# Performance work log

Measured on AMD Instinct MI355X. Metric: run time of the kernel, lower is better.

## Reference

```python
import jax, jax.numpy as jnp
import numpy as np

N, E, HN, K = 4096, 8192, 1024, 8
NF, EF = 128, 64
NH = [256, 256]
EH = [64, 64]
EMB = NH[-1] + len(EH)  # 258
BN_EPS = 1e-5


def setup_inputs() -> dict:
    key = jax.random.key(0)
    ks = jax.random.split(key, 16)

    def nrm(k, shape, fan):
        return jax.random.normal(k, shape, jnp.float32) / np.float32(np.sqrt(fan))

    return {
        "X_n": jax.random.normal(ks[0], (N, NF), jnp.float32),
        "X_e": jax.random.normal(ks[1], (E, EF), jnp.float32),
        # row-normalized-ish adjacency and scaled Laplacian to keep activations bounded
        "A_tilde": jax.random.uniform(ks[2], (N, N), jnp.float32) / np.float32(N),
        "L1_tilde": jax.random.normal(ks[3], (E, E), jnp.float32) / np.float32(np.sqrt(E)),
        "B1": jax.random.normal(ks[4], (N, E), jnp.float32) / np.float32(np.sqrt(E)),
        # GNN params (Linear stores weight as [out, in])
        "gnn_W1": nrm(ks[5], (NH[0], NF), NF), "gnn_b1": jnp.zeros((NH[0],), jnp.float32),
        "gnn_W2": nrm(ks[6], (NH[1], NH[0]), NH[0]), "gnn_b2": jnp.zeros((NH[1],), jnp.float32),
        # HoSC layer 1: in=EF, out=EH[0]
        "hosc_W1": nrm(ks[7], (EH[0], EF), EF), "hosc_b1": jnp.zeros((EH[0],), jnp.float32),
        "bn1_g": jnp.ones((EH[0],), jnp.float32), "bn1_b": jnp.zeros((EH[0],), jnp.float32),
        # HoSC layer 2: in=1 (after channel-max), out=EH[1]
        "hosc_W2": nrm(ks[8], (EH[1], 1), 1), "hosc_b2": jnp.zeros((EH[1],), jnp.float32),
        "bn2_g": jnp.ones((EH[1],), jnp.float32), "bn2_b": jnp.zeros((EH[1],), jnp.float32),
        # heads
        "node_W": nrm(ks[9], (1, EMB), EMB), "node_b": jnp.zeros((1,), jnp.float32),
        "edge_W": nrm(ks[10], (1, len(EH)), len(EH)), "edge_b": jnp.zeros((1,), jnp.float32),
        "hyper_W": nrm(ks[11], (1, EMB), EMB), "hyper_b": jnp.zeros((1,), jnp.float32),
        "hyperedges": jax.random.randint(ks[12], (HN, K), 0, N, jnp.int64),
    }


def _bn(x, g, b):
    # training-mode BatchNorm1d: biased batch statistics over rows
    m = jnp.mean(x, axis=0)
    v = jnp.var(x, axis=0)
    return g * (x - m) / jnp.sqrt(v + BN_EPS) + b


def _hosc_layer(Z, L1, W, bias, g, b):
    Zt = Z @ W.T + bias            # [E, out]
    Zc = L1 @ Zt                   # [E, out]
    Zp = jax.nn.relu(_bn(Zc, g, b))
    return jnp.max(Zp, axis=1, keepdims=True)  # [E, 1]


def reference(X_n, X_e, A_tilde, L1_tilde, B1,
              gnn_W1, gnn_b1, gnn_W2, gnn_b2,
              hosc_W1, hosc_b1, bn1_g, bn1_b,
              hosc_W2, hosc_b2, bn2_g, bn2_b,
              node_W, node_b, edge_W, edge_b, hyper_W, hyper_b,
              hyperedges):
    # --- GNN over nodes ---
    H = jax.nn.relu((A_tilde @ X_n) @ gnn_W1.T + gnn_b1)   # [N, 256]
    H_n = jax.nn.relu((A_tilde @ H) @ gnn_W2.T + gnn_b2)   # [N, 256]

    # --- HoSC over edges ---
    Z1 = _hosc_layer(X_e, L1_tilde, hosc_W1, hosc_b1, bn1_g, bn1_b)  # [E, 1]
    Z2 = _hosc_layer(Z1, L1_tilde, hosc_W2, hosc_b2, bn2_g, bn2_b)   # [E, 1]
    Z_H = jnp.concatenate([Z1, Z2], axis=1)                 # [E, 2]

    # --- fuse edge info into nodes ---
    H_e = B1 @ Z_H                                          # [N, 2]
    Hcat = jnp.concatenate([H_n, H_e], axis=1)              # [N, 258]

    node_prob = jax.nn.sigmoid(Hcat @ node_W.T + node_b).squeeze(-1)  # [N]
    edge_prob = jax.nn.sigmoid(Z_H @ edge_W.T + edge_b).squeeze(-1)   # [E]

    # vectorized hyperedge gather-mean-linear-sigmoid (fixed-size hyperedges)
    hfeat = Hcat[hyperedges].mean(axis=1)                   # [HN, 258]
    hyperedge_prob = jax.nn.sigmoid(hfeat @ hyper_W.T + hyper_b)  # [HN, 1]

    return node_prob, edge_prob, hyperedge_prob, Hcat
```

## Files before the change

kernel.cpp:

```cpp
#include <hip/hip_runtime.h>
#include <hip/hip_bf16.h>

using f32x4  = __attribute__((ext_vector_type(4))) float;
using u32x4  = __attribute__((ext_vector_type(4))) unsigned int;
using bf16x8 = __attribute__((ext_vector_type(8))) short;

__device__ __forceinline__ ushort f2bf(float x) {
    union { __hip_bfloat16 h; ushort u; } cv;
    cv.h = __float2bfloat16(x);
    return cv.u;
}
__device__ __forceinline__ unsigned pk2(float lo, float hi) {
    return (unsigned)f2bf(lo) | ((unsigned)f2bf(hi) << 16);
}
__device__ __forceinline__ float sigmoidf_(float x) { return 1.f / (1.f + expf(-x)); }

template<int NSUM, bool A_BF16, bool ABR, bool SPLIT, bool RELU, bool BF16_OUT, bool HAS_BIAS>
__device__ __forceinline__ void gemm_body(
    ushort* As, ushort* Bs,
    const void* __restrict__ Avoid, const ushort* __restrict__ B,
    const float* __restrict__ abias, const float* __restrict__ bias,
    float* __restrict__ Cf, ushort* __restrict__ Cb,
    int M, int N, int K, int ldc, int kPerChunk, long pStride,
    int bx, int by, int bz)
{
    const int tid  = threadIdx.x;
    const int lane = tid & 63;
    const int wid  = tid >> 6;
    const int wr   = wid >> 1, wc = wid & 1;
    const int g    = lane >> 4, lr = lane & 15;
    const long m0  = (long)bx * 128;
    const int  n0  = by * 64;

    int kbeg = 0, kend = K;
    if (SPLIT) { kbeg = bz * kPerChunk; kend = kbeg + kPerChunk; if (kend > K) kend = K; }

    const int bkr = tid & 31;
    const int bcb = tid >> 5;

    const float*  Af = (const float*)Avoid;
    const ushort* Ab = (const ushort*)Avoid;

    f32x4 pa[4];
    u32x4 pab[2];
    u32x4 pb;

    auto loadT = [&](int k0) {
        if (A_BF16) {
#pragma unroll
            for (int i = 0; i < 2; i++) {
                int s = tid + 256 * i; int row = s >> 2, c8 = s & 3;
                pab[i] = *(const u32x4*)(Ab + (m0 + row) * (long)K + k0 + c8 * 8);
            }
        } else {
#pragma unroll
            for (int i = 0; i < 4; i++) {
                int s = tid + 256 * i; int row = s >> 3, c4 = s & 7;
                const float* base = Af + (m0 + row) * (long)K + k0 + c4 * 4;
                f32x4 v = *(const f32x4*)base;
                if (NSUM > 0) {
#pragma unroll
                    for (int z = 1; z < NSUM; z++) v += *(const f32x4*)(base + z * pStride);
                }
                if (ABR) {
                    f32x4 bq = *(const f32x4*)(abias + k0 + c4 * 4);
                    v.x = fmaxf(v.x + bq.x, 0.f);
                    v.y = fmaxf(v.y + bq.y, 0.f);
                    v.z = fmaxf(v.z + bq.z, 0.f);
                    v.w = fmaxf(v.w + bq.w, 0.f);
                }
                pa[i] = v;
            }
        }
        pb = *(const u32x4*)(B + (long)(k0 + bkr) * N + n0 + bcb * 8);
    };
    auto storeT = [&]() {
        if (A_BF16) {
#pragma unroll
            for (int i = 0; i < 2; i++) {
                int s = tid + 256 * i; int row = s >> 2, c8 = s & 3;
                *(u32x4*)(&As[row * 40 + c8 * 8]) = pab[i];
            }
        } else {
#pragma unroll
            for (int i = 0; i < 4; i++) {
                int s = tid + 256 * i; int row = s >> 3, c4 = s & 7;
                ushort4 w;
                w.x = f2bf(pa[i].x); w.y = f2bf(pa[i].y);
                w.z = f2bf(pa[i].z); w.w = f2bf(pa[i].w);
                *(ushort4*)(&As[row * 40 + c4 * 4]) = w;
            }
        }
        const ushort* p8 = (const ushort*)&pb;
#pragma unroll
        for (int j = 0; j < 8; j++) Bs[(bcb * 8 + j) * 40 + bkr] = p8[j];
    };

    f32x4 acc[4][2] = {};

    const int nk = (kend - kbeg) >> 5;
    loadT(kbeg);
    for (int t = 0; t < nk; ++t) {
        storeT();
        __syncthreads();
        if (t + 1 < nk) loadT(kbeg + ((t + 1) << 5));
        bf16x8 af[4], bfr[2];
#pragma unroll
        for (int fm = 0; fm < 4; fm++)
            af[fm] = *(const bf16x8*)(&As[(wr * 64 + fm * 16 + lr) * 40 + g * 8]);
#pragma unroll
        for (int fn = 0; fn < 2; fn++)
            bfr[fn] = *(const bf16x8*)(&Bs[(wc * 32 + fn * 16 + lr) * 40 + g * 8]);
#pragma unroll
        for (int fm = 0; fm < 4; fm++)
#pragma unroll
            for (int fn = 0; fn < 2; fn++)
                acc[fm][fn] = __builtin_amdgcn_mfma_f32_16x16x32_bf16(af[fm], bfr[fn], acc[fm][fn], 0, 0, 0);
        __syncthreads();
    }

    if (SPLIT) {
        float* P = Cf + (long)bz * M * N;
#pragma unroll
        for (int fm = 0; fm < 4; fm++)
#pragma unroll
            for (int fn = 0; fn < 2; fn++)
#pragma unroll
                for (int rr = 0; rr < 4; rr++) {
                    long row = m0 + wr * 64 + fm * 16 + g * 4 + rr;
                    int  col = n0 + wc * 32 + fn * 16 + lr;
                    P[row * N + col] = acc[fm][fn][rr];
                }
    } else {
#pragma unroll
        for (int fm = 0; fm < 4; fm++)
#pragma unroll
            for (int fn = 0; fn < 2; fn++)
#pragma unroll
                for (int rr = 0; rr < 4; rr++) {
                    long row = m0 + wr * 64 + fm * 16 + g * 4 + rr;
                    int  col = n0 + wc * 32 + fn * 16 + lr;
                    float v = acc[fm][fn][rr];
                    if (HAS_BIAS) v += bias[col];
                    if (RELU) v = fmaxf(v, 0.f);
                    if (BF16_OUT) Cb[row * ldc + col] = f2bf(v);
                    else          Cf[row * ldc + col] = v;
                }
    }
}

__global__ __launch_bounds__(256)
void prep_k(const float* __restrict__ A, ushort* __restrict__ Abf,
            const float* __restrict__ Xn, const float* __restrict__ W1, ushort* __restrict__ T1,
            const float* __restrict__ Xe, const float* __restrict__ Wh,
            const float* __restrict__ hb, ushort* __restrict__ Zt1,
            const float* __restrict__ W2, ushort* __restrict__ W2t,
            float* __restrict__ stats)
{
    __shared__ float xs[1024];
    int b = blockIdx.x, t = threadIdx.x;
    if (b < 8192) {
        long j = (long)b * 256 + t;
        f32x4 v0 = ((const f32x4*)A)[2 * j];
        f32x4 v1 = ((const f32x4*)A)[2 * j + 1];
        u32x4 w;
        w.x = pk2(v0.x, v0.y); w.y = pk2(v0.z, v0.w);
        w.z = pk2(v1.x, v1.y); w.w = pk2(v1.z, v1.w);
        ((u32x4*)Abf)[j] = w;
    } else if (b < 8704) {
        int r0 = (b - 8192) * 8;
        for (int idx = t; idx < 1024; idx += 256) xs[idx] = Xn[(long)r0 * 128 + idx];
        __syncthreads();
        float acc[8] = {};
        const float* wrow = W1 + (long)t * 128;
        for (int i = 0; i < 128; i++) {
            float w = wrow[i];
#pragma unroll
            for (int r = 0; r < 8; r++) acc[r] += xs[r * 128 + i] * w;
        }
#pragma unroll
        for (int r = 0; r < 8; r++) T1[(long)(r0 + r) * 256 + t] = f2bf(acc[r]);
    } else if (b < 10752) {
        int row = (b - 8704) * 4 + (t >> 6);
        int o   = t & 63;
        const float* xr = Xe + (long)row * 64;
        const float* wr = Wh + (long)o * 64;
        float acc = hb[o];
#pragma unroll 8
        for (int i = 0; i < 64; i++) acc += xr[i] * wr[i];
        Zt1[(long)row * 64 + o] = f2bf(acc);
    } else if (b < 11008) {
        int j = (b - 10752) * 256 + t;
        int i = j >> 8, o = j & 255;
        W2t[j] = f2bf(W2[o * 256 + i]);
    } else {
        if (t < 256) stats[t] = 0.f;
    }
}

__device__ __forceinline__ void bnred_body(int b, const float* __restrict__ P,
                                           float* __restrict__ Zc,
                                           float* __restrict__ pstats,
                                           float* __restrict__ gsum, float* __restrict__ gsq,
                                           unsigned* __restrict__ ctr)
{
    const long MN = 8192 * 64;
    int t = threadIdx.x;
    int c = t & 63, rg = t >> 6;
    float sx = 0.f, sq = 0.f;
    int base = b * 32 + rg;
#pragma unroll 4
    for (int i = 0; i < 8; i++) {
        long idx = (long)(base + 4 * i) * 64 + c;
        float x = 0.f;
#pragma unroll
        for (int z = 0; z < 8; z++) x += P[idx + z * MN];
        Zc[idx] = x;
        sx += x; sq += x * x;
    }
    __shared__ float ls[256], lq[256];
    ls[t] = sx; lq[t] = sq;
    __syncthreads();
    if (t < 64) {
        float a = ls[t] + ls[t + 64] + ls[t + 128] + ls[t + 192];
        float q = lq[t] + lq[t + 64] + lq[t + 128] + lq[t + 192];
        pstats[b * 128 + t]      = a;
        pstats[b * 128 + 64 + t] = q;
    }
    __threadfence();
    __syncthreads();
    __shared__ unsigned lastflag;
    if (t == 0) {
        unsigned old = atomicAdd(ctr, 1u);
        lastflag = (old == 255u);
    }
    __syncthreads();
    if (lastflag) {
        __threadfence();
        if (t < 128) {
            float a = 0.f;
            for (int bb = 0; bb < 256; bb++) a += pstats[bb * 128 + t];
            if (t < 64) gsum[t] = a;
            else        gsq[t - 64] = a;
        }
    }
}

__device__ __forceinline__ void z1_body(int b, const float* __restrict__ Zc,
                                        const float* __restrict__ gsum, const float* __restrict__ gsq,
                                        const float* __restrict__ g, const float* __restrict__ bb,
                                        float* __restrict__ Z1)
{
    int w = threadIdx.x >> 6, lane = threadIdx.x & 63;
    int row = b * 4 + w;
    const float inv = 1.f / 8192.f;
    float m = gsum[lane] * inv;
    float v = gsq[lane] * inv - m * m;
    float x = Zc[row * 64 + lane];
    float y = fmaxf(g[lane] * (x - m) * rsqrtf(v + 1e-5f) + bb[lane], 0.f);
#pragma unroll
    for (int o = 32; o > 0; o >>= 1) y = fmaxf(y, __shfl_xor(y, o));
    if (lane == 0) Z1[row] = y;
}

__device__ __forceinline__ void pass2_body(int row, const float* __restrict__ L1,
                                           const float* __restrict__ Z1,
                                           float* __restrict__ s, float* __restrict__ r)
{
    int t = threadIdx.x;
    int l = t & 63, w = t >> 6;
    const f32x4* rp = (const f32x4*)(L1 + (long)row * 8192);
    const f32x4* z4 = (const f32x4*)Z1;
    float as = 0.f, ar = 0.f;
#pragma unroll 4
    for (int k = 0; k < 8; k++) {
        f32x4 v = rp[t + 256 * k];
        f32x4 z = z4[t + 256 * k];
        as += v.x * z.x + v.y * z.y + v.z * z.z + v.w * z.w;
        ar += v.x + v.y + v.z + v.w;
    }
#pragma unroll
    for (int o = 32; o > 0; o >>= 1) { as += __shfl_xor(as, o); ar += __shfl_xor(ar, o); }
    __shared__ float sw[4], rw[4];
    if (l == 0) { sw[w] = as; rw[w] = ar; }
    __syncthreads();
    if (t == 0) {
        s[row] = sw[0] + sw[1] + sw[2] + sw[3];
        r[row] = rw[0] + rw[1] + rw[2] + rw[3];
    }
}

__device__ __forceinline__ void hcatred_body(int b, const float* __restrict__ P,
                                             const float* __restrict__ b2, float* __restrict__ hcat)
{
    const long MNq = (long)4096 * 256 / 4;
    int j = b * 256 + threadIdx.x;
    int row = j >> 6, c4 = (j & 63) * 4;
    const f32x4* Q = (const f32x4*)P;
    f32x4 v = Q[j] + Q[j + MNq] + Q[j + 2 * MNq] + Q[j + 3 * MNq];
    f32x4 bq = *(const f32x4*)(b2 + c4);
    float* dst = hcat + (long)row * 258 + c4;
    float2 lo = { fmaxf(v.x + bq.x, 0.f), fmaxf(v.y + bq.y, 0.f) };
    float2 hi = { fmaxf(v.z + bq.z, 0.f), fmaxf(v.w + bq.w, 0.f) };
    *(float2*)dst = lo;
    *(float2*)(dst + 2) = hi;
}

__global__ __launch_bounds__(256)
void dual_a_k(const float* __restrict__ L1, const ushort* __restrict__ Zt1, float* __restrict__ Pa,
              const ushort* __restrict__ Abf, const ushort* __restrict__ T1, float* __restrict__ Pb)
{
    __shared__ ushort As[128 * 40];
    __shared__ ushort Bs[64 * 40];
    int bid = blockIdx.x;
    if (bid < 512) {
        gemm_body<0, false, false, true, false, false, false>(
            As, Bs, L1, Zt1, nullptr, nullptr, Pa, nullptr,
            8192, 64, 8192, 64, 1024, 0, bid & 63, 0, bid >> 6);
    } else {
        int b = bid - 512;
        gemm_body<0, true, false, true, false, false, false>(
            As, Bs, Abf, T1, nullptr, nullptr, Pb, nullptr,
            4096, 256, 4096, 256, 1024, 0, b & 31, (b >> 5) & 3, b >> 7);
    }
}

__global__ __launch_bounds__(256)
void dual_b_k(const float* __restrict__ Pb, const float* __restrict__ gb1,
              const ushort* __restrict__ W2t, ushort* __restrict__ T2,
              const float* __restrict__ Pa, float* __restrict__ Zc1,
              float* __restrict__ pstats,
              float* __restrict__ gsum, float* __restrict__ gsq, unsigned* __restrict__ ctr)
{
    __shared__ ushort As[128 * 40];
    __shared__ ushort Bs[64 * 40];
    int bid = blockIdx.x;
    if (bid < 128) {
        gemm_body<4, false, true, false, false, true, false>(
            As, Bs, Pb, W2t, gb1, nullptr, nullptr, T2,
            4096, 256, 256, 256, 0, (long)4096 * 256, bid & 31, bid >> 5, 0);
    } else {
        bnred_body(bid - 128, Pa, Zc1, pstats, gsum, gsq, ctr);
    }
}

__global__ __launch_bounds__(256)
void dual_c_k(const ushort* __restrict__ Abf, const ushort* __restrict__ T2, float* __restrict__ Pa,
              const float* __restrict__ Zc1, const float* __restrict__ gsum,
              const float* __restrict__ gsq, const float* __restrict__ bn1g,
              const float* __restrict__ bn1b, float* __restrict__ Z1)
{
    __shared__ ushort As[128 * 40];
    __shared__ ushort Bs[64 * 40];
    int bid = blockIdx.x;
    if (bid < 512) {
        gemm_body<0, true, false, true, false, false, false>(
            As, Bs, Abf, T2, nullptr, nullptr, Pa, nullptr,
            4096, 256, 4096, 256, 1024, 0, bid & 31, (bid >> 5) & 3, bid >> 7);
    } else {
        z1_body(bid - 512, Zc1, gsum, gsq, bn1g, bn1b, Z1);
    }
}

__global__ __launch_bounds__(256)
void dual_d_k(const float* __restrict__ Pa, const float* __restrict__ gb2, float* __restrict__ hcat,
              const float* __restrict__ L1, const float* __restrict__ Z1,
              float* __restrict__ s, float* __restrict__ r)
{
    int bid = blockIdx.x;
    if (bid < 1024) hcatred_body(bid, Pa, gb2, hcat);
    else            pass2_body(bid - 1024, L1, Z1, s, r);
}

__global__ __launch_bounds__(1024) void stats2_k(const float* __restrict__ s, const float* __restrict__ r,
                                                 float* __restrict__ S5)
{
    int t = threadIdx.x, l = t & 63, w = t >> 6;
    float Ss = 0, Sr = 0, Sss = 0, Srr = 0, Ssr = 0;
    for (int i = t; i < 8192; i += 1024) {
        float sv = s[i], rv = r[i];
        Ss += sv; Sr += rv; Sss += sv * sv; Srr += rv * rv; Ssr += sv * rv;
    }
#pragma unroll
    for (int o = 32; o > 0; o >>= 1) {
        Ss += __shfl_xor(Ss, o); Sr += __shfl_xor(Sr, o);
        Sss += __shfl_xor(Sss, o); Srr += __shfl_xor(Srr, o); Ssr += __shfl_xor(Ssr, o);
    }
    __shared__ float buf[16][5];
    if (l == 0) { buf[w][0] = Ss; buf[w][1] = Sr; buf[w][2] = Sss; buf[w][3] = Srr; buf[w][4] = Ssr; }
    __syncthreads();
    if (t < 5) {
        float a = 0.f;
#pragma unroll
        for (int i = 0; i < 16; i++) a += buf[i][t];
        S5[t] = a;
    }
}

__global__ __launch_bounds__(256) void z2_edge_k(const float* __restrict__ s, const float* __restrict__ r,
                                                 const float* __restrict__ S,
                                                 const float* __restrict__ W2, const float* __restrict__ b2,
                                                 const float* __restrict__ g2, const float* __restrict__ bb2,
                                                 const float* __restrict__ eW, const float* __restrict__ eb,
                                                 const float* __restrict__ Z1,
                                                 float* __restrict__ Z2, float* __restrict__ edge_out)
{
    int w = threadIdx.x >> 6, lane = threadIdx.x & 63;
    int row = blockIdx.x * 4 + w;
    const float inv = 1.f / 8192.f;
    float ms = S[0] * inv, mr = S[1] * inv;
    float vs = S[2] * inv - ms * ms;
    float vr = S[3] * inv - mr * mr;
    float cv = S[4] * inv - ms * mr;
    float w2 = W2[lane], bz = b2[lane];
    float mc = w2 * ms + bz * mr;
    float vc = w2 * w2 * vs + 2.f * w2 * bz * cv + bz * bz * vr;
    float x  = w2 * s[row] + bz * r[row];
    float y  = fmaxf(g2[lane] * (x - mc) * rsqrtf(vc + 1e-5f) + bb2[lane], 0.f);
#pragma unroll
    for (int o = 32; o > 0; o >>= 1) y = fmaxf(y, __shfl_xor(y, o));
    if (lane == 0) {
        Z2[row] = y;
        float e = Z1[row] * eW[0] + y * eW[1] + eb[0];
        edge_out[row] = sigmoidf_(e);
    }
}

__global__ __launch_bounds__(256) void he_node_k(const float* __restrict__ B1, const float* __restrict__ Z1,
                                                 const float* __restrict__ Z2, float* __restrict__ hcat,
                                                 const float* __restrict__ nW, const float* __restrict__ nb,
                                                 float* __restrict__ node_out)
{
    int n = blockIdx.x, t = threadIdx.x;
    int l = t & 63, w = t >> 6;
    const f32x4* rp  = (const f32x4*)(B1 + (long)n * 8192);
    const f32x4* z1v = (const f32x4*)Z1;
    const f32x4* z2v = (const f32x4*)Z2;
    float a1 = 0.f, a2 = 0.f;
#pragma unroll 4
    for (int k = 0; k < 8; k++) {
        f32x4 v = rp[t + 256 * k];
        f32x4 p = z1v[t + 256 * k];
        f32x4 q = z2v[t + 256 * k];
        a1 += v.x * p.x + v.y * p.y + v.z * p.z + v.w * p.w;
        a2 += v.x * q.x + v.y * q.y + v.z * q.z + v.w * q.w;
    }
    float d = hcat[(long)n * 258 + t] * nW[t];
#pragma unroll
    for (int o = 32; o > 0; o >>= 1) {
        a1 += __shfl_xor(a1, o); a2 += __shfl_xor(a2, o); d += __shfl_xor(d, o);
    }
    __shared__ float s1[4], s2[4], s3[4];
    if (l == 0) { s1[w] = a1; s2[w] = a2; s3[w] = d; }
    __syncthreads();
    if (t == 0) {
        float A1 = s1[0] + s1[1] + s1[2] + s1[3];
        float A2 = s2[0] + s2[1] + s2[2] + s2[3];
        float D  = s3[0] + s3[1] + s3[2] + s3[3];
        hcat[(long)n * 258 + 256] = A1;
        hcat[(long)n * 258 + 257] = A2;
        node_out[n] = sigmoidf_(D + A1 * nW[256] + A2 * nW[257] + nb[0]);
    }
}

__global__ __launch_bounds__(256) void hyper_k(const void* __restrict__ he_idx,
                                               const float* __restrict__ hcat,
                                               const float* __restrict__ hW, const float* __restrict__ hb,
                                               float* __restrict__ out)
{
    int w = threadIdx.x >> 6, lane = threadIdx.x & 63;
    int h = blockIdx.x * 4 + w;
    const unsigned int* u = (const unsigned int*)he_idx;
    unsigned int odd = u[2 * lane + 1];
    bool is64 = __all(odd == 0u);
    float acc = 0.f;
    for (int k = 0; k < 8; k++) {
        int idx;
        if (is64) idx = (int)((const long long*)he_idx)[h * 8 + k];
        else      idx = ((const int*)he_idx)[h * 8 + k];
        const float* hr = hcat + (long)idx * 258;
        for (int d = lane; d < 258; d += 64) acc += hr[d] * hW[d];
    }
    acc *= 0.125f;
#pragma unroll
    for (int o = 32; o > 0; o >>= 1) acc += __shfl_xor(acc, o);
    if (lane == 0) out[h] = sigmoidf_(acc + hb[0]);
}

extern "C" void kernel_launch(void* const* d_in, const int* in_sizes, int n_in,
                              void* d_out, int out_size, void* d_ws, size_t ws_size,
                              hipStream_t stream)
{
    const float* X_n  = (const float*)d_in[0];
    const float* X_e  = (const float*)d_in[1];
    const float* A_t  = (const float*)d_in[2];
    const float* L1   = (const float*)d_in[3];
    const float* B1   = (const float*)d_in[4];
    const float* gW1  = (const float*)d_in[5];
    const float* gb1  = (const float*)d_in[6];
    const float* gW2  = (const float*)d_in[7];
    const float* gb2  = (const float*)d_in[8];
    const float* hW1  = (const float*)d_in[9];
    const float* hb1  = (const float*)d_in[10];
    const float* bn1g = (const float*)d_in[11];
    const float* bn1b = (const float*)d_in[12];
    const float* hW2  = (const float*)d_in[13];
    const float* hb2  = (const float*)d_in[14];
    const float* bn2g = (const float*)d_in[15];
    const float* bn2b = (const float*)d_in[16];
    const float* nW   = (const float*)d_in[17];
    const float* nb   = (const float*)d_in[18];
    const float* eW   = (const float*)d_in[19];
    const float* ebb  = (const float*)d_in[20];
    const float* yW   = (const float*)d_in[21];
    const float* yb   = (const float*)d_in[22];
    const void*  he   = d_in[23];

    float* out       = (float*)d_out;
    float* out_node  = out;
    float* out_edge  = out + 4096;
    float* out_hyper = out + 12288;
    float* hcat      = out + 13312;

    size_t off = 0;
    auto alloc = [&](size_t bytes) {
        void* p = (char*)d_ws + off;
        off = (off + bytes + 255) & ~(size_t)255;
        return p;
    };
    ushort* Abf    = (ushort*)alloc((size_t)4096 * 4096 * 2);
    ushort* T1     = (ushort*)alloc(4096 * 256 * 2);
    ushort* T2     = (ushort*)alloc(4096 * 256 * 2);
    ushort* Zt1    = (ushort*)alloc(8192 * 64 * 2);
    ushort* W2t    = (ushort*)alloc(256 * 256 * 2);
    float*  Zc1    = (float*)alloc(8192 * 64 * 4);
    float*  stats  = (float*)alloc(256 * 4);
    float*  gsum   = stats;
    float*  gsq    = stats + 64;
    float*  S5     = stats + 128;
    unsigned* ctr  = (unsigned*)(stats + 192);
    float*  pstats = (float*)alloc(256 * 128 * 4);
    float*  Z1     = (float*)alloc(8192 * 4);
    float*  Z2     = (float*)alloc(8192 * 4);
    float*  sbuf   = (float*)alloc(8192 * 4);
    float*  rbuf   = (float*)alloc(8192 * 4);
    float*  Pa     = (float*)alloc((size_t)8192 * 64 * 8 * 4);
    float*  Pb     = (float*)alloc((size_t)4096 * 256 * 4 * 4);

    prep_k<<<11009, 256, 0, stream>>>(A_t, Abf, X_n, gW1, T1, X_e, hW1, hb1, Zt1,
                                      gW2, W2t, stats);

    dual_a_k<<<1024, 256, 0, stream>>>(L1, Zt1, Pa, Abf, T1, Pb);

    dual_b_k<<<384, 256, 0, stream>>>(Pb, gb1, W2t, T2, Pa, Zc1, pstats, gsum, gsq, ctr);

    dual_c_k<<<2560, 256, 0, stream>>>(Abf, T2, Pa, Zc1, gsum, gsq, bn1g, bn1b, Z1);

    dual_d_k<<<9216, 256, 0, stream>>>(Pa, gb2, hcat, L1, Z1, sbuf, rbuf);

    stats2_k<<<1, 1024, 0, stream>>>(sbuf, rbuf, S5);

    z2_edge_k<<<2048, 256, 0, stream>>>(sbuf, rbuf, S5, hW2, hb2, bn2g, bn2b,
                                        eW, ebb, Z1, Z2, out_edge);

    he_node_k<<<4096, 256, 0, stream>>>(B1, Z1, Z2, hcat, nW, nb, out_node);

    hyper_k<<<256, 256, 0, stream>>>(he, hcat, yW, yb, out_hyper);
}
```

Baseline: 311.3 us.

## Stream L1 GEMM straight from global memory and replace last-block reduction with atomics

The L1_tilde @ Zt1 split-K GEMM no longer stages tiles through LDS. Each lane loads fp32 L1 rows straight into registers, converts them to bf16 in place, and reads a transposed Zt1 layout written by prep_k, then feeds MFMA directly. This removes shared-memory staging and barriers from the largest fp32 read. The BatchNorm statistics reduction now uses atomicAdd into gsum and gsq instead of per-block partials plus a last-block fold, which makes the summation order nondeterministic. Uncoalesced row-strided global loads with no reuse across waves may hurt bandwidth.

```diff
diff --git a/kernel.cpp b/kernel.cpp
--- a/kernel.cpp
+++ b/kernel.cpp
@@ -149,11 +149,70 @@
     }
 }
 
+__device__ __forceinline__ void k6_nolds_body(
+    const float* __restrict__ L1, const ushort* __restrict__ Zt1T,
+    float* __restrict__ Pa, int bx, int bz)
+{
+    const int tid  = threadIdx.x;
+    const int lane = tid & 63;
+    const int wid  = tid >> 6;
+    const int wr   = wid >> 1, wc = wid & 1;
+    const int g    = lane >> 4, lr = lane & 15;
+    const long K   = 8192;
+    const int kbeg = bz * 1024;
+
+    const float* arow[4];
+#pragma unroll
+    for (int fm = 0; fm < 4; fm++)
+        arow[fm] = L1 + (long)(bx * 128 + wr * 64 + fm * 16 + lr) * K + g * 8;
+    const ushort* brow[2];
+#pragma unroll
+    for (int fn = 0; fn < 2; fn++)
+        brow[fn] = Zt1T + (long)(wc * 32 + fn * 16 + lr) * K + g * 8;
+
+    f32x4 acc[4][2] = {};
+
+#pragma unroll 2
+    for (int kt = 0; kt < 32; ++kt) {
+        int k0 = kbeg + kt * 32;
+        bf16x8 af[4], bf[2];
+#pragma unroll
+        for (int fm = 0; fm < 4; fm++) {
+            const f32x4* ap = (const f32x4*)(arow[fm] + k0);
+            f32x4 a0 = ap[0], a1 = ap[1];
+            union { u32x4 u; bf16x8 b; } cv;
+            cv.u.x = pk2(a0.x, a0.y); cv.u.y = pk2(a0.z, a0.w);
+            cv.u.z = pk2(a1.x, a1.y); cv.u.w = pk2(a1.z, a1.w);
+            af[fm] = cv.b;
+        }
+#pragma unroll
+        for (int fn = 0; fn < 2; fn++)
+            bf[fn] = *(const bf16x8*)(brow[fn] + k0);
+#pragma unroll
+        for (int fm = 0; fm < 4; fm++)
+#pragma unroll
+            for (int fn = 0; fn < 2; fn++)
+                acc[fm][fn] = __builtin_amdgcn_mfma_f32_16x16x32_bf16(af[fm], bf[fn], acc[fm][fn], 0, 0, 0);
+    }
+
+    float* P = Pa + (long)bz * 8192 * 64;
+#pragma unroll
+    for (int fm = 0; fm < 4; fm++)
+#pragma unroll
+        for (int fn = 0; fn < 2; fn++)
+#pragma unroll
+            for (int rr = 0; rr < 4; rr++) {
+                long row = (long)bx * 128 + wr * 64 + fm * 16 + g * 4 + rr;
+                int  col = wc * 32 + fn * 16 + lr;
+                P[row * 64 + col] = acc[fm][fn][rr];
+            }
+}
+
 __global__ __launch_bounds__(256)
 void prep_k(const float* __restrict__ A, ushort* __restrict__ Abf,
             const float* __restrict__ Xn, const float* __restrict__ W1, ushort* __restrict__ T1,
             const float* __restrict__ Xe, const float* __restrict__ Wh,
-            const float* __restrict__ hb, ushort* __restrict__ Zt1,
+            const float* __restrict__ hb, ushort* __restrict__ Zt1T,
             const float* __restrict__ W2, ushort* __restrict__ W2t,
             float* __restrict__ stats)
 {
@@ -188,7 +247,7 @@
         float acc = hb[o];
 #pragma unroll 8
         for (int i = 0; i < 64; i++) acc += xr[i] * wr[i];
-        Zt1[(long)row * 64 + o] = f2bf(acc);
+        Zt1T[(long)o * 8192 + row] = f2bf(acc);
     } else if (b < 11008) {
         int j = (b - 10752) * 256 + t;
         int i = j >> 8, o = j & 255;
@@ -200,9 +259,7 @@
 
 __device__ __forceinline__ void bnred_body(int b, const float* __restrict__ P,
                                            float* __restrict__ Zc,
-                                           float* __restrict__ pstats,
-                                           float* __restrict__ gsum, float* __restrict__ gsq,
-                                           unsigned* __restrict__ ctr)
+                                           float* __restrict__ gsum, float* __restrict__ gsq)
 {
     const long MN = 8192 * 64;
     int t = threadIdx.x;
@@ -224,25 +281,8 @@
     if (t < 64) {
         float a = ls[t] + ls[t + 64] + ls[t + 128] + ls[t + 192];
         float q = lq[t] + lq[t + 64] + lq[t + 128] + lq[t + 192];
-        pstats[b * 128 + t]      = a;
-        pstats[b * 128 + 64 + t] = q;
-    }
-    __threadfence();
-    __syncthreads();
-    __shared__ unsigned lastflag;
-    if (t == 0) {
-        unsigned old = atomicAdd(ctr, 1u);
-        lastflag = (old == 255u);
-    }
-    __syncthreads();
-    if (lastflag) {
-        __threadfence();
-        if (t < 128) {
-            float a = 0.f;
-            for (int bb = 0; bb < 256; bb++) a += pstats[bb * 128 + t];
-            if (t < 64) gsum[t] = a;
-            else        gsq[t - 64] = a;
-        }
+        atomicAdd(&gsum[t], a);
+        atomicAdd(&gsq[t], q);
     }
 }
 
@@ -307,16 +347,14 @@
 }
 
 __global__ __launch_bounds__(256)
-void dual_a_k(const float* __restrict__ L1, const ushort* __restrict__ Zt1, float* __restrict__ Pa,
+void dual_a_k(const float* __restrict__ L1, const ushort* __restrict__ Zt1T, float* __restrict__ Pa,
               const ushort* __restrict__ Abf, const ushort* __restrict__ T1, float* __restrict__ Pb)
 {
     __shared__ ushort As[128 * 40];
     __shared__ ushort Bs[64 * 40];
     int bid = blockIdx.x;
     if (bid < 512) {
-        gemm_body<0, false, false, true, false, false, false>(
-            As, Bs, L1, Zt1, nullptr, nullptr, Pa, nullptr,
-            8192, 64, 8192, 64, 1024, 0, bid & 63, 0, bid >> 6);
+        k6_nolds_body(L1, Zt1T, Pa, bid & 63, bid >> 6);
     } else {
         int b = bid - 512;
         gemm_body<0, true, false, true, false, false, false>(
@@ -329,8 +367,7 @@
 void dual_b_k(const float* __restrict__ Pb, const float* __restrict__ gb1,
               const ushort* __restrict__ W2t, ushort* __restrict__ T2,
               const float* __restrict__ Pa, float* __restrict__ Zc1,
-              float* __restrict__ pstats,
-              float* __restrict__ gsum, float* __restrict__ gsq, unsigned* __restrict__ ctr)
+              float* __restrict__ gsum, float* __restrict__ gsq)
 {
     __shared__ ushort As[128 * 40];
     __shared__ ushort Bs[64 * 40];
@@ -340,7 +377,7 @@
             As, Bs, Pb, W2t, gb1, nullptr, nullptr, T2,
             4096, 256, 256, 256, 0, (long)4096 * 256, bid & 31, bid >> 5, 0);
     } else {
-        bnred_body(bid - 128, Pa, Zc1, pstats, gsum, gsq, ctr);
+        bnred_body(bid - 128, Pa, Zc1, gsum, gsq);
     }
 }
 
@@ -531,15 +568,13 @@
     ushort* Abf    = (ushort*)alloc((size_t)4096 * 4096 * 2);
     ushort* T1     = (ushort*)alloc(4096 * 256 * 2);
     ushort* T2     = (ushort*)alloc(4096 * 256 * 2);
-    ushort* Zt1    = (ushort*)alloc(8192 * 64 * 2);
+    ushort* Zt1T   = (ushort*)alloc(8192 * 64 * 2);
     ushort* W2t    = (ushort*)alloc(256 * 256 * 2);
     float*  Zc1    = (float*)alloc(8192 * 64 * 4);
     float*  stats  = (float*)alloc(256 * 4);
     float*  gsum   = stats;
     float*  gsq    = stats + 64;
     float*  S5     = stats + 128;
-    unsigned* ctr  = (unsigned*)(stats + 192);
-    float*  pstats = (float*)alloc(256 * 128 * 4);
     float*  Z1     = (float*)alloc(8192 * 4);
     float*  Z2     = (float*)alloc(8192 * 4);
     float*  sbuf   = (float*)alloc(8192 * 4);
@@ -547,12 +582,12 @@
     float*  Pa     = (float*)alloc((size_t)8192 * 64 * 8 * 4);
     float*  Pb     = (float*)alloc((size_t)4096 * 256 * 4 * 4);
 
-    prep_k<<<11009, 256, 0, stream>>>(A_t, Abf, X_n, gW1, T1, X_e, hW1, hb1, Zt1,
+    prep_k<<<11009, 256, 0, stream>>>(A_t, Abf, X_n, gW1, T1, X_e, hW1, hb1, Zt1T,
                                       gW2, W2t, stats);
 
-    dual_a_k<<<1024, 256, 0, stream>>>(L1, Zt1, Pa, Abf, T1, Pb);
-
-    dual_b_k<<<384, 256, 0, stream>>>(Pb, gb1, W2t, T2, Pa, Zc1, pstats, gsum, gsq, ctr);
+    dual_a_k<<<1024, 256, 0, stream>>>(L1, Zt1T, Pa, Abf, T1, Pb);
+
+    dual_b_k<<<384, 256, 0, stream>>>(Pb, gb1, W2t, T2, Pa, Zc1, gsum, gsq);
 
     dual_c_k<<<2560, 256, 0, stream>>>(Abf, T2, Pa, Zc1, gsum, gsq, bn1g, bn1b, Z1);
 
```

Result: slower. 321.8 us (+3.4%).
